# Kernel tuning notes

Hardware: AMD Instinct MI355X
Metric: run time of the kernel (lower is better)

The kernel has to match this reference:

```python
import jax, jax.numpy as jnp
import numpy as np

WS, WS2, UP = 8, 16, 2
DIM, HEADS = 192, 6
HD = DIM // HEADS
SCALE = HD ** -0.5
EPS = 1e-5

def _rel_index():
    r1, c1 = np.meshgrid(np.arange(WS), np.arange(WS), indexing='ij')
    r2, c2 = np.meshgrid(np.arange(WS2), np.arange(WS2), indexing='ij')
    r1, c1 = r1.ravel(), c1.ravel()          # 64 query positions
    r2, c2 = r2.ravel(), c2.ravel()          # 256 kv positions
    rel_row = r1[:, None] - r2[None, :]
    rel_col = c1[:, None] - c2[None, :]
    off = WS * UP - 1    # 15
    span = WS + WS * UP - 1  # 23
    return jnp.asarray((rel_row + off) * span + (rel_col + off))  # (64, 256)

REL_IDX = _rel_index()

def layer_norm(x, w, b):
    m = x.mean(-1, keepdims=True)
    v = ((x - m) ** 2).mean(-1, keepdims=True)
    return (x - m) * jax.lax.rsqrt(v + EPS) * w + b

def window_partition(x, ws):
    B, H, W, C = x.shape
    x = x.reshape(B, H // ws, ws, W // ws, ws, C).transpose(0, 1, 3, 2, 4, 5)
    return x.reshape(-1, ws * ws, C)

def window_reverse(w, ws, H, W, B):
    x = w.reshape(B, H // ws, W // ws, ws, ws, -1).transpose(0, 1, 3, 2, 4, 5)
    return x.reshape(B, H, W, -1)

def setup_inputs() -> dict:
    key = jax.random.key(0)
    ks = jax.random.split(key, 8)
    B, H, W, H2, W2 = 4, 128, 128, 256, 256
    s = 0.02
    return {
        'x': jax.random.normal(ks[0], (B, H * W, DIM), jnp.float32),
        'x2': jax.random.normal(ks[1], (B, H2 * W2, DIM), jnp.float32),
        'norm1_w': jnp.ones((DIM,), jnp.float32),
        'norm1_b': jnp.zeros((DIM,), jnp.float32),
        'qkv_w': jax.random.normal(ks[2], (DIM, DIM), jnp.float32) * s,
        'qkv_b': jnp.zeros((DIM,), jnp.float32),
        'qkv2_w': jax.random.normal(ks[3], (2 * DIM, DIM), jnp.float32) * s,
        'qkv2_b': jnp.zeros((2 * DIM,), jnp.float32),
        'rel_bias': jax.random.normal(ks[4], (23 * 23, HEADS), jnp.float32) * s,
        'proj_w': jax.random.normal(ks[5], (DIM, DIM), jnp.float32) * s,
        'proj_b': jnp.zeros((DIM,), jnp.float32),
        'norm2_w': jnp.ones((DIM,), jnp.float32),
        'norm2_b': jnp.zeros((DIM,), jnp.float32),
        'fc1_w': jax.random.normal(ks[6], (4 * DIM, DIM), jnp.float32) * s,
        'fc1_b': jnp.zeros((4 * DIM,), jnp.float32),
        'fc2_w': jax.random.normal(ks[7], (DIM, 4 * DIM), jnp.float32) * s,
        'fc2_b': jnp.zeros((DIM,), jnp.float32),
        'H': 128, 'W': 128, 'H2': 256, 'W2': 256,
    }

def reference(x, x2, norm1_w, norm1_b, qkv_w, qkv_b, qkv2_w, qkv2_b, rel_bias,
              proj_w, proj_b, norm2_w, norm2_b, fc1_w, fc1_b, fc2_w, fc2_b,
              H, W, H2, W2):
    B, L, C = x.shape
    shortcut = x
    xn = layer_norm(x, norm1_w, norm1_b).reshape(B, H, W, C)
    x2r = x2.reshape(B, H2, W2, C)

    xw = window_partition(xn, WS)      # (nW, 64, C)
    x2w = window_partition(x2r, WS2)   # (nW, 256, C)

    q = (xw @ qkv_w.T + qkv_b).reshape(-1, WS * WS, HEADS, HD).transpose(0, 2, 1, 3)
    kv = (x2w @ qkv2_w.T + qkv2_b).reshape(-1, WS2 * WS2, 2, HEADS, HD).transpose(2, 0, 3, 1, 4)
    k, v = kv[0], kv[1]                # (nW, h, 256, d)

    attn = jnp.einsum('whnd,whmd->whnm', q * SCALE, k)   # (nW, h, 64, 256)
    bias = rel_bias[REL_IDX]                             # (64, 256, h)
    attn = attn + bias.transpose(2, 0, 1)[None]
    attn = jax.nn.softmax(attn, axis=-1)
    out = jnp.einsum('whnm,whmd->wnhd', attn, v).reshape(-1, WS * WS, C)
    out = out @ proj_w.T + proj_b

    x = shortcut + window_reverse(out, WS, H, W, B).reshape(B, H * W, C)
    h = layer_norm(x, norm2_w, norm2_b)
    h = jax.nn.gelu(h @ fc1_w.T + fc1_b, approximate=False)
    x = x + (h @ fc2_w.T + fc2_b)
    return x
```

## Files before the change

kernel.cpp:

```cpp
#include <hip/hip_runtime.h>
#include <hip/hip_bf16.h>
#include <math.h>

typedef unsigned int u32;
typedef unsigned short u16;

typedef __attribute__((ext_vector_type(8))) short bf16x8;
typedef __attribute__((ext_vector_type(4))) float f32x4;

__device__ __forceinline__ float bflo(u32 u){ union{u32 i; float f;} c; c.i = u << 16; return c.f; }
__device__ __forceinline__ float bfhi(u32 u){ union{u32 i; float f;} c; c.i = u & 0xffff0000u; return c.f; }
__device__ __forceinline__ float bfs(u16 s){ union{u32 i; float f;} c; c.i = ((u32)s) << 16; return c.f; }
__device__ __forceinline__ u32 packbf(float a, float b){
  union{float f; u32 i;} ca, cb; ca.f = a; cb.f = b;
  u32 ua = (ca.i + 0x7fffu + ((ca.i >> 16) & 1u)) >> 16;
  u32 ub = (cb.i + 0x7fffu + ((cb.i >> 16) & 1u)) >> 16;
  return (ua & 0xffffu) | (ub << 16);
}
__device__ __forceinline__ u16 bf1(float a){
  union{float f; u32 i;} c; c.f = a;
  return (u16)((c.i + 0x7fffu + ((c.i >> 16) & 1u)) >> 16);
}
__device__ __forceinline__ bf16x8 pack8(float f0,float f1,float f2,float f3,
                                        float f4,float f5,float f6,float f7){
  union { u32 u[4]; bf16x8 v; } cv;
  cv.u[0]=packbf(f0,f1); cv.u[1]=packbf(f2,f3); cv.u[2]=packbf(f4,f5); cv.u[3]=packbf(f6,f7);
  return cv.v;
}
__device__ __forceinline__ float gelu_exact(float v){ return 0.5f*v*(1.0f + erff(v*0.70710678118654752f)); }
__device__ __forceinline__ bool detect_f32(const u32* rawn1){ return (rawn1[0] & 0xFFFFu) == 0u; }

#define SCALE_Q 0.17677669529663687f

#define P_N1W 0
#define P_N1B 192
#define P_N2W 384
#define P_N2B 576
#define P_QKVB 768
#define P_QKV2B 960
#define P_PROJB 1344
#define P_FC1B 1536
#define P_FC2B 2304
#define P_RELB 2496
#define P_TOTAL 5670
#define W_QKV 0
#define W_QKV2 18432
#define W_PROJ 55296
#define W_FC1 73728
#define W_FC2 147456
#define W_TOTAL 221184

__device__ __forceinline__ void stage_w64x192(const u32* __restrict__ src, u32* lds, int tid){
  #pragma unroll
  for (int t = 0; t < 6; ++t) {
    int idx = tid + t*256;
    int j = idx / 24, seg = idx % 24;
    uint4 v = *(const uint4*)(src + (size_t)j*96 + seg*4);
    int byt = (j*384 + seg*16) ^ ((j&7)<<4);
    *(uint4*)((char*)lds + byt) = v;
  }
}
__device__ __forceinline__ void stage_w64x192_t512(const u32* __restrict__ src, u32* lds, int tid){
  #pragma unroll
  for (int t = 0; t < 3; ++t) {
    int idx = tid + t*512;
    int j = idx / 24, seg = idx % 24;
    uint4 v = *(const uint4*)(src + (size_t)j*96 + seg*4);
    int byt = (j*384 + seg*16) ^ ((j&7)<<4);
    *(uint4*)((char*)lds + byt) = v;
  }
}
__device__ __forceinline__ void stage_w192x64_t512(const u32* __restrict__ src, int ch, u32* lds, int tid){
  #pragma unroll
  for (int t = 0; t < 3; ++t) {
    int idx = tid + t*512;
    int j = idx / 8, seg = idx % 8;
    uint4 v = *(const uint4*)(src + (size_t)j*384 + ch*32 + seg*4);
    int byt = (j*128 + seg*16) ^ ((j&7)<<4);
    *(uint4*)((char*)lds + byt) = v;
  }
}
__device__ __forceinline__ bf16x8 lds_w64(const u32* lds, int j, int kt, int g){
  int byt = (j*384 + kt*64 + g*16) ^ ((j&7)<<4);
  return *(const bf16x8*)((const char*)lds + byt);
}
__device__ __forceinline__ bf16x8 lds_w192(const u32* lds, int j, int kk, int g){
  int byt = (j*128 + kk*64 + g*16) ^ ((j&7)<<4);
  return *(const bf16x8*)((const char*)lds + byt);
}

__global__ __launch_bounds__(256) void k_canon_w(
    const void* qkvw, const void* qkv2w, const void* projw,
    const void* fc1w, const void* fc2w, const u32* rawn1, u32* cw)
{
  int idx = blockIdx.x*256 + threadIdx.x;
  bool isf32 = detect_f32(rawn1);
  const void* src; int off;
  if      (idx < W_QKV2){ src=qkvw;  off=idx; }
  else if (idx < W_PROJ){ src=qkv2w; off=idx-W_QKV2; }
  else if (idx < W_FC1) { src=projw; off=idx-W_PROJ; }
  else if (idx < W_FC2) { src=fc1w;  off=idx-W_FC1; }
  else                  { src=fc2w;  off=idx-W_FC2; }
  u32 o;
  if (isf32) { float2 v = ((const float2*)src)[off]; o = packbf(v.x, v.y); }
  else       { o = ((const u32*)src)[off]; }
  cw[idx] = o;
}

__global__ __launch_bounds__(256) void k_canon_v(
    const void* n1w, const void* n1b, const void* n2w, const void* n2b,
    const void* qkvb, const void* qkv2b, const void* projb,
    const void* fc1b, const void* fc2b, const void* relb,
    const u32* rawn1, float* par)
{
  int idx = blockIdx.x*256 + threadIdx.x;
  if (idx >= P_TOTAL) return;
  bool isf32 = detect_f32(rawn1);
  const void* src; int off;
  if      (idx < P_N1B)  { src=n1w;  off=idx; }
  else if (idx < P_N2W)  { src=n1b;  off=idx-P_N1B; }
  else if (idx < P_N2B)  { src=n2w;  off=idx-P_N2W; }
  else if (idx < P_QKVB) { src=n2b;  off=idx-P_N2B; }
  else if (idx < P_QKV2B){ src=qkvb; off=idx-P_QKVB; }
  else if (idx < P_PROJB){ src=qkv2b;off=idx-P_QKV2B; }
  else if (idx < P_FC1B) { src=projb;off=idx-P_PROJB; }
  else if (idx < P_FC2B) { src=fc1b; off=idx-P_FC1B; }
  else if (idx < P_RELB) { src=fc2b; off=idx-P_FC2B; }
  else                   { src=relb; off=idx-P_RELB; }
  par[idx] = isf32 ? ((const float*)src)[off] : bfs(((const u16*)src)[off]);
}

__global__ __launch_bounds__(256) void k_bias(
    const float* __restrict__ par, float* __restrict__ tbl)
{
  int idx = blockIdx.x*256 + threadIdx.x;
  int h  = idx >> 12;
  int remi = idx & 4095;
  int kt = remi >> 8;
  int qt = (remi >> 6) & 3;
  int ll = idx & 63;
  int lr = ll & 15, g = ll >> 4;
  int q = qt*16 + lr;
  int r1 = q >> 3, c1 = q & 7;
  float vv[4];
  #pragma unroll
  for (int i = 0; i < 4; ++i) {
    int kv = kt*16 + 4*g + i;
    int r2 = kv >> 4, c2 = kv & 15;
    vv[i] = par[P_RELB + ((r1-r2+15)*23 + (c1-c2+15))*6 + h];
  }
  ((float4*)tbl)[idx] = make_float4(vv[0], vv[1], vv[2], vv[3]);
}

__global__ __launch_bounds__(256) void k_qproj(
    const void* __restrict__ x, const u32* __restrict__ rawn1,
    const u32* __restrict__ cw, const float* __restrict__ par,
    u16* __restrict__ q_ws)
{
  __shared__ u32 wbuf[6144];
  int tid = threadIdx.x;
  int l = tid & 63, w = tid >> 6, lr = l & 15, g = l >> 4;
  int wi = blockIdx.x;
  int b = wi >> 8, rem = wi & 255, wh = rem >> 4, ww = rem & 15;
  bool isf32 = detect_f32(rawn1);

  bf16x8 a[6];
  {
    int t = w*16 + lr;
    int r = t >> 3, c = t & 7;
    size_t grow = (size_t)b*16384 + (size_t)(wh*8+r)*128 + (ww*8+c);
    float4 xf[12];
    if (isf32) {
      const float* xp = (const float*)x + grow*192;
      #pragma unroll
      for (int kt = 0; kt < 6; ++kt) {
        xf[kt*2]   = *(const float4*)(xp + kt*32 + 8*g);
        xf[kt*2+1] = *(const float4*)(xp + kt*32 + 8*g + 4);
      }
    } else {
      const u32* xp = (const u32*)x + grow*96;
      #pragma unroll
      for (int kt = 0; kt < 6; ++kt) {
        uint4 u = *(const uint4*)(xp + kt*16 + 4*g);
        xf[kt*2]   = make_float4(bflo(u.x), bfhi(u.x), bflo(u.y), bfhi(u.y));
        xf[kt*2+1] = make_float4(bflo(u.z), bfhi(u.z), bflo(u.w), bfhi(u.w));
      }
    }
    float s = 0.f, s2 = 0.f;
    #pragma unroll
    for (int q8 = 0; q8 < 12; ++q8) {
      s  += xf[q8].x + xf[q8].y + xf[q8].z + xf[q8].w;
      s2 += xf[q8].x*xf[q8].x + xf[q8].y*xf[q8].y + xf[q8].z*xf[q8].z + xf[q8].w*xf[q8].w;
    }
    s += __shfl_xor(s, 16); s2 += __shfl_xor(s2, 16);
    s += __shfl_xor(s, 32); s2 += __shfl_xor(s2, 32);
    float m = s * (1.f/192.f);
    float rstd = rsqrtf(s2*(1.f/192.f) - m*m + 1e-5f);
    #pragma unroll
    for (int kt = 0; kt < 6; ++kt) {
      int k0 = kt*32 + 8*g;
      float4 w0 = *(const float4*)(par + P_N1W + k0);
      float4 w1 = *(const float4*)(par + P_N1W + k0 + 4);
      float4 b0 = *(const float4*)(par + P_N1B + k0);
      float4 b1 = *(const float4*)(par + P_N1B + k0 + 4);
      float4 f0 = xf[kt*2], f1 = xf[kt*2+1];
      a[kt] = pack8((f0.x-m)*rstd*w0.x + b0.x, (f0.y-m)*rstd*w0.y + b0.y,
                    (f0.z-m)*rstd*w0.z + b0.z, (f0.w-m)*rstd*w0.w + b0.w,
                    (f1.x-m)*rstd*w1.x + b1.x, (f1.y-m)*rstd*w1.y + b1.y,
                    (f1.z-m)*rstd*w1.z + b1.z, (f1.w-m)*rstd*w1.w + b1.w);
    }
  }

  for (int ch = 0; ch < 3; ++ch) {
    __syncthreads();
    stage_w64x192(cw + W_QKV + (size_t)(ch*64)*96, wbuf, tid);
    __syncthreads();
    #pragma unroll
    for (int nt2 = 0; nt2 < 4; ++nt2) {
      int j = ch*64 + nt2*16 + lr;
      f32x4 acc = {0.f,0.f,0.f,0.f};
      #pragma unroll
      for (int kt = 0; kt < 6; ++kt) {
        bf16x8 bb = lds_w64(wbuf, nt2*16 + lr, kt, g);
        acc = __builtin_amdgcn_mfma_f32_16x16x32_bf16(a[kt], bb, acc, 0, 0, 0);
      }
      float bj = par[P_QKVB + j];
      int h = j >> 5, d = j & 31;
      #pragma unroll
      for (int i = 0; i < 4; ++i) {
        int n = w*16 + 4*g + i;
        q_ws[(size_t)(wi*6+h)*2048 + (size_t)n*32 + d] = bf1((acc[i] + bj) * SCALE_Q);
      }
    }
  }
}

__global__ __launch_bounds__(256) void k_kvproj(
    const void* __restrict__ x2, const u32* __restrict__ rawn1,
    const u32* __restrict__ cw, const float* __restrict__ par,
    u16* __restrict__ k_ws, u16* __restrict__ v_ws, int win0)
{
  __shared__ u32 wbuf[6144];
  int tid = threadIdx.x;
  int l = tid & 63, w = tid >> 6, lr = l & 15, g = l >> 4;
  int lwi = blockIdx.x >> 2, sub = blockIdx.x & 3;
  int wi = win0 + lwi;
  int b = wi >> 8, rem = wi & 255, wh = rem >> 4, ww = rem & 15;
  bool isf32 = detect_f32(rawn1);

  bf16x8 a[6];
  {
    int tt = sub*64 + w*16 + lr;
    int r = tt >> 4, c = tt & 15;
    size_t grow = (size_t)b*65536 + (size_t)(wh*16+r)*256 + (ww*16+c);
    if (isf32) {
      const float4* xp = (const float4*)x2 + grow*48;
      #pragma unroll
      for (int kt = 0; kt < 6; ++kt) {
        float4 f0 = xp[kt*8 + g*2];
        float4 f1 = xp[kt*8 + g*2 + 1];
        a[kt] = pack8(f0.x,f0.y,f0.z,f0.w, f1.x,f1.y,f1.z,f1.w);
      }
    } else {
      const u32* xp = (const u32*)x2 + grow*96;
      #pragma unroll
      for (int kt = 0; kt < 6; ++kt)
        a[kt] = *(const bf16x8*)(xp + kt*16 + g*4);
    }
  }

  for (int ch = 0; ch < 6; ++ch) {
    __syncthreads();
    stage_w64x192(cw + W_QKV2 + (size_t)(ch*64)*96, wbuf, tid);
    __syncthreads();
    if (ch < 3) {
      #pragma unroll
      for (int nt2 = 0; nt2 < 4; ++nt2) {
        int j = ch*64 + nt2*16 + lr;
        f32x4 acc = {0.f,0.f,0.f,0.f};
        #pragma unroll
        for (int kt = 0; kt < 6; ++kt) {
          bf16x8 bb = lds_w64(wbuf, nt2*16 + lr, kt, g);
          acc = __builtin_amdgcn_mfma_f32_16x16x32_bf16(a[kt], bb, acc, 0, 0, 0);
        }
        float bj = par[P_QKV2B + j];
        int h = j >> 5, d = j & 31;
        u16* dst = k_ws + (size_t)(lwi*6 + h)*8192 + d;
        #pragma unroll
        for (int i = 0; i < 4; ++i) {
          int tok = sub*64 + w*16 + 4*g + i;
          dst[(size_t)tok*32] = bf1(acc[i] + bj);
        }
      }
    } else {
      #pragma unroll
      for (int nt2 = 0; nt2 < 4; ++nt2) {
        f32x4 acc = {0.f,0.f,0.f,0.f};
        #pragma unroll
        for (int kt = 0; kt < 6; ++kt) {
          bf16x8 bb = lds_w64(wbuf, nt2*16 + lr, kt, g);
          acc = __builtin_amdgcn_mfma_f32_16x16x32_bf16(bb, a[kt], acc, 0, 0, 0);
        }
        int jr0 = (ch-3)*64 + nt2*16 + 4*g;
        int tok = sub*64 + w*16 + lr;
        #pragma unroll
        for (int i = 0; i < 4; ++i) {
          int jp = jr0 + i;
          int h = jp >> 5, dd = jp & 31;
          v_ws[(size_t)(lwi*6 + h)*8192 + (size_t)dd*256 + tok] = bf1(acc[i] + par[P_QKV2B + 192 + jp]);
        }
      }
    }
  }
}

__global__ __launch_bounds__(256) void k_attn(
    const u16* __restrict__ q_ws, const u16* __restrict__ k_ws,
    const u16* __restrict__ v_ws, const float* __restrict__ tbl,
    u16* __restrict__ O_ws, int win0)
{
  __shared__ u32 Psh[4*1024];
  __shared__ float msh[2][2][4];
  int tid = threadIdx.x;
  int w = tid >> 6, l = tid & 63;
  int lr = l & 15, g = l >> 4;
  int pairi = w >> 1, half = w & 1;
  int task = blockIdx.x*2 + pairi;
  int lwi = task / 6, h = task - lwi*6;
  int wi = win0 + lwi;

  bf16x8 qb[4];
  {
    const u16* qp = q_ws + (size_t)(wi*6+h)*2048;
    #pragma unroll
    for (int qt = 0; qt < 4; ++qt)
      qb[qt] = *(const bf16x8*)(qp + (qt*16 + lr)*32 + 8*g);
  }
  const u16* kp = k_ws + (size_t)(lwi*6+h)*8192;
  const u16* vp = v_ws + (size_t)(lwi*6+h)*8192;
  const float4* tb4 = (const float4*)tbl + (size_t)h*4096 + l;

  f32x4 ao[2][4];
  #pragma unroll
  for (int dt = 0; dt < 2; ++dt)
    #pragma unroll
    for (int qt = 0; qt < 4; ++qt) ao[dt][qt] = (f32x4){0.f,0.f,0.f,0.f};
  float mreg[4] = {-3.0e38f,-3.0e38f,-3.0e38f,-3.0e38f};
  float sreg[4] = {0.f,0.f,0.f,0.f};
  u32* pbu = Psh + w*1024;

  for (int ch = half*4; ch < half*4 + 4; ++ch) {
    bf16x8 ka0 = *(const bf16x8*)(kp + (2*ch)*512   + lr*32 + 8*g);
    bf16x8 ka1 = *(const bf16x8*)(kp + (2*ch+1)*512 + lr*32 + 8*g);
    f32x4 s0[4], s1[4];
    #pragma unroll
    for (int qt = 0; qt < 4; ++qt) {
      float4 b0 = tb4[(2*ch)*256   + qt*64];
      float4 b1 = tb4[(2*ch+1)*256 + qt*64];
      f32x4 c0; c0[0]=b0.x; c0[1]=b0.y; c0[2]=b0.z; c0[3]=b0.w;
      f32x4 c1; c1[0]=b1.x; c1[1]=b1.y; c1[2]=b1.z; c1[3]=b1.w;
      s0[qt] = __builtin_amdgcn_mfma_f32_16x16x32_bf16(ka0, qb[qt], c0, 0, 0, 0);
      s1[qt] = __builtin_amdgcn_mfma_f32_16x16x32_bf16(ka1, qb[qt], c1, 0, 0, 0);
    }
    #pragma unroll
    for (int qt = 0; qt < 4; ++qt) {
      float pm = fmaxf(fmaxf(fmaxf(s0[qt][0],s0[qt][1]), fmaxf(s0[qt][2],s0[qt][3])),
                       fmaxf(fmaxf(s1[qt][0],s1[qt][1]), fmaxf(s1[qt][2],s1[qt][3])));
      pm = fmaxf(pm, __shfl_xor(pm, 16));
      pm = fmaxf(pm, __shfl_xor(pm, 32));
      float nm = fmaxf(mreg[qt], pm);
      float resc = __expf(mreg[qt] - nm);
      mreg[qt] = nm;
      float p00 = __expf(s0[qt][0]-nm), p01 = __expf(s0[qt][1]-nm),
            p02 = __expf(s0[qt][2]-nm), p03 = __expf(s0[qt][3]-nm);
      float p10 = __expf(s1[qt][0]-nm), p11 = __expf(s1[qt][1]-nm),
            p12 = __expf(s1[qt][2]-nm), p13 = __expf(s1[qt][3]-nm);
      float ps = ((p00+p01)+(p02+p03)) + ((p10+p11)+(p12+p13));
      ps += __shfl_xor(ps, 16);
      ps += __shfl_xor(ps, 32);
      sreg[qt] = sreg[qt]*resc + ps;
      #pragma unroll
      for (int dt = 0; dt < 2; ++dt) {
        ao[dt][qt][0] *= resc; ao[dt][qt][1] *= resc;
        ao[dt][qt][2] *= resc; ao[dt][qt][3] *= resc;
      }
      int row = qt*16 + lr;
      int sw = (row & 3) << 2;
      *(uint2*)&pbu[row*16 + ((2*g) ^ sw)]     = make_uint2(packbf(p00,p01), packbf(p02,p03));
      *(uint2*)&pbu[row*16 + ((8 + 2*g) ^ sw)] = make_uint2(packbf(p10,p11), packbf(p12,p13));
    }
    asm volatile("" ::: "memory");
    bf16x8 va0 = *(const bf16x8*)(vp + lr*256        + ch*32 + 8*g);
    bf16x8 va1 = *(const bf16x8*)(vp + (16 + lr)*256 + ch*32 + 8*g);
    #pragma unroll
    for (int qt = 0; qt < 4; ++qt) {
      int row = qt*16 + lr;
      int sw = (row & 3) << 2;
      bf16x8 pa = *(const bf16x8*)&pbu[row*16 + ((4*g) ^ sw)];
      ao[0][qt] = __builtin_amdgcn_mfma_f32_16x16x32_bf16(va0, pa, ao[0][qt], 0, 0, 0);
      ao[1][qt] = __builtin_amdgcn_mfma_f32_16x16x32_bf16(va1, pa, ao[1][qt], 0, 0, 0);
    }
    asm volatile("" ::: "memory");
  }

  __syncthreads();
  if (half == 1) {
    float* dst = (float*)(Psh + pairi*2048);
    #pragma unroll
    for (int dt = 0; dt < 2; ++dt)
      #pragma unroll
      for (int qt = 0; qt < 4; ++qt)
        #pragma unroll
        for (int i = 0; i < 4; ++i)
          dst[(dt*16 + qt*4 + i)*64 + l] = ao[dt][qt][i];
    if (l == 0) {
      msh[pairi][0][0] = mreg[0]; msh[pairi][0][1] = mreg[1];
      msh[pairi][0][2] = mreg[2]; msh[pairi][0][3] = mreg[3];
      msh[pairi][1][0] = sreg[0]; msh[pairi][1][1] = sreg[1];
      msh[pairi][1][2] = sreg[2]; msh[pairi][1][3] = sreg[3];
    }
  }
  __syncthreads();
  if (half == 0) {
    const float* src = (const float*)(Psh + pairi*2048);
    #pragma unroll
    for (int qt = 0; qt < 4; ++qt) {
      float m1 = msh[pairi][0][qt], s1 = msh[pairi][1][qt];
      float M = fmaxf(mreg[qt], m1);
      float e0 = __expf(mreg[qt] - M), e1 = __expf(m1 - M);
      float rs = 1.0f / (sreg[qt]*e0 + s1*e1);
      u16* orow = O_ws + ((size_t)(wi*64) + qt*16 + lr)*192 + h*32;
      #pragma unroll
      for (int dt = 0; dt < 2; ++dt)
        #pragma unroll
        for (int i = 0; i < 4; ++i) {
          float o = ao[dt][qt][i]*e0 + src[(dt*16 + qt*4 + i)*64 + l]*e1;
          orow[dt*16 + 4*g + i] = bf1(o * rs);
        }
    }
  }
}

__global__ __launch_bounds__(256) void k_proj(
    const u16* __restrict__ O_ws, const u32* __restrict__ cw,
    const float* __restrict__ par, const void* __restrict__ x,
    const u32* __restrict__ rawn1, float* __restrict__ xres)
{
  __shared__ u32 wbuf[6144];
  int wi = blockIdx.x;
  int b = wi >> 8, rem = wi & 255, wh = rem >> 4, ww = rem & 15;
  int tid = threadIdx.x;
  int l = tid & 63, w = tid >> 6, lr = l & 15, g = l >> 4;
  bool isf32 = detect_f32(rawn1);
  int t = w*16 + lr;
  const u16* op = O_ws + (size_t)(wi*64 + t)*192;
  bf16x8 a[6];
  #pragma unroll
  for (int kt = 0; kt < 6; ++kt) a[kt] = *(const bf16x8*)(op + kt*32 + 8*g);

  for (int ch = 0; ch < 3; ++ch) {
    __syncthreads();
    stage_w64x192(cw + W_PROJ + (size_t)(ch*64)*96, wbuf, tid);
    __syncthreads();
    #pragma unroll
    for (int nt2 = 0; nt2 < 4; ++nt2) {
      int j = ch*64 + nt2*16 + lr;
      f32x4 acc = {0.f,0.f,0.f,0.f};
      #pragma unroll
      for (int kt = 0; kt < 6; ++kt) {
        bf16x8 bb = lds_w64(wbuf, nt2*16 + lr, kt, g);
        acc = __builtin_amdgcn_mfma_f32_16x16x32_bf16(a[kt], bb, acc, 0, 0, 0);
      }
      float bj = par[P_PROJB + j];
      #pragma unroll
      for (int i = 0; i < 4; ++i) {
        int tok = w*16 + 4*g + i;
        int rr = tok >> 3, cc = tok & 7;
        size_t grow = (size_t)b*16384 + (size_t)(wh*8+rr)*128 + (ww*8+cc);
        float sres = isf32 ? ((const float*)x)[grow*192 + j]
                           : bfs(((const u16*)x)[grow*192 + j]);
        xres[grow*192 + j] = sres + acc[i] + bj;
      }
    }
  }
}

__global__ __launch_bounds__(512) void k_mlp(
    const float* __restrict__ xres, const u32* __restrict__ cw,
    const float* __restrict__ par, float* __restrict__ out)
{
  __shared__ u32 wbuf[6144];
  __shared__ u16 Hc[8][32][64];
  int tid = threadIdx.x;
  int l = tid & 63, w = tid >> 6;
  int lr = l & 15, g = l >> 4;
  size_t row0 = (size_t)blockIdx.x * 256;

  bf16x8 a[2][6];
  #pragma unroll
  for (int mt = 0; mt < 2; ++mt) {
    size_t t = row0 + w*32 + mt*16 + lr;
    const float* xr = xres + t*192;
    float4 xf[12];
    #pragma unroll
    for (int kt = 0; kt < 6; ++kt) {
      xf[kt*2]   = *(const float4*)(xr + kt*32 + 8*g);
      xf[kt*2+1] = *(const float4*)(xr + kt*32 + 8*g + 4);
    }
    float s = 0.f, s2 = 0.f;
    #pragma unroll
    for (int q = 0; q < 12; ++q) {
      s  += xf[q].x + xf[q].y + xf[q].z + xf[q].w;
      s2 += xf[q].x*xf[q].x + xf[q].y*xf[q].y + xf[q].z*xf[q].z + xf[q].w*xf[q].w;
    }
    s += __shfl_xor(s, 16); s2 += __shfl_xor(s2, 16);
    s += __shfl_xor(s, 32); s2 += __shfl_xor(s2, 32);
    float m = s * (1.f/192.f);
    float rstd = rsqrtf(s2*(1.f/192.f) - m*m + 1e-5f);
    #pragma unroll
    for (int kt = 0; kt < 6; ++kt) {
      int k0 = kt*32 + 8*g;
      float4 w0 = *(const float4*)(par + P_N2W + k0);
      float4 w1 = *(const float4*)(par + P_N2W + k0 + 4);
      float4 b0 = *(const float4*)(par + P_N2B + k0);
      float4 b1 = *(const float4*)(par + P_N2B + k0 + 4);
      float4 f0 = xf[kt*2], f1 = xf[kt*2+1];
      a[mt][kt] = pack8((f0.x-m)*rstd*w0.x + b0.x, (f0.y-m)*rstd*w0.y + b0.y,
                        (f0.z-m)*rstd*w0.z + b0.z, (f0.w-m)*rstd*w0.w + b0.w,
                        (f1.x-m)*rstd*w1.x + b1.x, (f1.y-m)*rstd*w1.y + b1.y,
                        (f1.z-m)*rstd*w1.z + b1.z, (f1.w-m)*rstd*w1.w + b1.w);
    }
  }

  f32x4 acc2[2][12];
  #pragma unroll
  for (int mt = 0; mt < 2; ++mt)
    #pragma unroll
    for (int i = 0; i < 12; ++i) acc2[mt][i] = (f32x4){0.f,0.f,0.f,0.f};

  char* hbase = (char*)&Hc[w][0][0];
  for (int ch = 0; ch < 12; ++ch) {
    __syncthreads();
    stage_w64x192_t512(cw + W_FC1 + (size_t)(ch*64)*96, wbuf, tid);
    __syncthreads();
    #pragma unroll
    for (int nt2 = 0; nt2 < 4; ++nt2) {
      f32x4 acc0 = {0.f,0.f,0.f,0.f}, acc1 = {0.f,0.f,0.f,0.f};
      #pragma unroll
      for (int kt = 0; kt < 6; ++kt) {
        bf16x8 bb = lds_w64(wbuf, nt2*16 + lr, kt, g);
        acc0 = __builtin_amdgcn_mfma_f32_16x16x32_bf16(a[0][kt], bb, acc0, 0, 0, 0);
        acc1 = __builtin_amdgcn_mfma_f32_16x16x32_bf16(a[1][kt], bb, acc1, 0, 0, 0);
      }
      float bj = par[P_FC1B + ch*64 + nt2*16 + lr];
      #pragma unroll
      for (int mt = 0; mt < 2; ++mt) {
        f32x4 acc = mt ? acc1 : acc0;
        #pragma unroll
        for (int i = 0; i < 4; ++i) {
          int row = mt*16 + 4*g + i;
          int byt = (row*128 + (nt2*16+lr)*2) ^ ((row&7)<<4);
          *(u16*)(hbase + byt) = bf1(gelu_exact(acc[i] + bj));
        }
      }
    }
    __syncthreads();
    stage_w192x64_t512(cw + W_FC2, ch, wbuf, tid);
    __syncthreads();
    #pragma unroll
    for (int kk = 0; kk < 2; ++kk) {
      bf16x8 a20, a21;
      {
        int row0h = lr, row1h = 16 + lr;
        a20 = *(const bf16x8*)(hbase + ((row0h*128 + kk*64 + g*16) ^ ((row0h&7)<<4)));
        a21 = *(const bf16x8*)(hbase + ((row1h*128 + kk*64 + g*16) ^ ((row1h&7)<<4)));
      }
      #pragma unroll
      for (int nt = 0; nt < 12; ++nt) {
        bf16x8 bb = lds_w192(wbuf, nt*16 + lr, kk, g);
        acc2[0][nt] = __builtin_amdgcn_mfma_f32_16x16x32_bf16(a20, bb, acc2[0][nt], 0, 0, 0);
        acc2[1][nt] = __builtin_amdgcn_mfma_f32_16x16x32_bf16(a21, bb, acc2[1][nt], 0, 0, 0);
      }
    }
  }

  #pragma unroll
  for (int mt = 0; mt < 2; ++mt) {
    size_t trow = row0 + w*32 + mt*16 + 4*g;
    #pragma unroll
    for (int nt = 0; nt < 12; ++nt) {
      int j = nt*16 + lr;
      float bj = par[P_FC2B + j];
      #pragma unroll
      for (int i = 0; i < 4; ++i)
        out[(trow+i)*192 + j] = xres[(trow+i)*192 + j] + acc2[mt][nt][i] + bj;
    }
  }
}

extern "C" void kernel_launch(void* const* d_in, const int* in_sizes, int n_in,
                              void* d_out, int out_size, void* d_ws, size_t ws_size,
                              hipStream_t stream) {
  const void* x      = d_in[0];
  const void* x2     = d_in[1];
  const void* n1w    = d_in[2];
  const void* n1b    = d_in[3];
  const void* qkv_w  = d_in[4];
  const void* qkv_b  = d_in[5];
  const void* qkv2_w = d_in[6];
  const void* qkv2_b = d_in[7];
  const void* relb   = d_in[8];
  const void* proj_w = d_in[9];
  const void* proj_b = d_in[10];
  const void* n2w    = d_in[11];
  const void* n2b    = d_in[12];
  const void* fc1_w  = d_in[13];
  const void* fc1_b  = d_in[14];
  const void* fc2_w  = d_in[15];
  const void* fc2_b  = d_in[16];
  const u32* rawn1   = (const u32*)d_in[2];
  float* out = (float*)d_out;

  int nslice = (ws_size >= 202700000ull) ? 2 : 4;
  int nw = 1024 / nslice;
  size_t kvb = (size_t)nw * 98304;

  char* ws = (char*)d_ws;
  u16*   q_ws = (u16*)ws;
  u16*   k_ws = (u16*)(ws + 25165824);
  u16*   v_ws = (u16*)(ws + 25165824 + kvb);
  u16*   O_ws = (u16*)(ws + 25165824 + 2*kvb);
  float* xres = (float*)(ws + 50331648 + 2*kvb);
  u32*   cw   = (u32*)(ws + 100663296 + 2*kvb);
  float* tbl  = (float*)(ws + 100663296 + 2*kvb + 884736);
  float* par  = (float*)(ws + 100663296 + 2*kvb + 884736 + 393216);

  k_canon_w<<<W_TOTAL/256, 256, 0, stream>>>(qkv_w, qkv2_w, proj_w, fc1_w, fc2_w, rawn1, cw);
  k_canon_v<<<(P_TOTAL+255)/256, 256, 0, stream>>>(n1w, n1b, n2w, n2b, qkv_b, qkv2_b,
                                                   proj_b, fc1_b, fc2_b, relb, rawn1, par);
  k_bias  <<<96, 256, 0, stream>>>(par, tbl);
  k_qproj <<<1024, 256, 0, stream>>>(x, rawn1, cw, par, q_ws);
  for (int s = 0; s < nslice; ++s) {
    int win0 = s*nw;
    k_kvproj<<<nw*4, 256, 0, stream>>>(x2, rawn1, cw, par, k_ws, v_ws, win0);
    k_attn  <<<nw*3, 256, 0, stream>>>(q_ws, k_ws, v_ws, tbl, O_ws, win0);
  }
  k_proj  <<<1024, 256, 0, stream>>>(O_ws, cw, par, x, rawn1, xres);
  k_mlp   <<< 256, 512, 0, stream>>>(xres, cw, par, out);
}
```

Before: 648.7 us.

## Double-buffer MLP weight chunks with async global-to-LDS loads

The MLP kernel now uses two LDS weight buffers and issues direct global-to-LDS loads (global_load_lds) so the fc2 chunk loads while fc1 MFMAs run, and the next fc1 chunk loads while fc2 MFMAs run. The swizzle is folded into the global address so the LDS layout stays the same. This removes two barriers per chunk and the register round trip of staging. It raises LDS use by 24KB, which may lower occupancy, and it relies on the barrier placement being enough to wait for the async loads to finish.

```diff
diff --git a/kernel.cpp b/kernel.cpp
--- a/kernel.cpp
+++ b/kernel.cpp
@@ -60,26 +60,6 @@
     *(uint4*)((char*)lds + byt) = v;
   }
 }
-__device__ __forceinline__ void stage_w64x192_t512(const u32* __restrict__ src, u32* lds, int tid){
-  #pragma unroll
-  for (int t = 0; t < 3; ++t) {
-    int idx = tid + t*512;
-    int j = idx / 24, seg = idx % 24;
-    uint4 v = *(const uint4*)(src + (size_t)j*96 + seg*4);
-    int byt = (j*384 + seg*16) ^ ((j&7)<<4);
-    *(uint4*)((char*)lds + byt) = v;
-  }
-}
-__device__ __forceinline__ void stage_w192x64_t512(const u32* __restrict__ src, int ch, u32* lds, int tid){
-  #pragma unroll
-  for (int t = 0; t < 3; ++t) {
-    int idx = tid + t*512;
-    int j = idx / 8, seg = idx % 8;
-    uint4 v = *(const uint4*)(src + (size_t)j*384 + ch*32 + seg*4);
-    int byt = (j*128 + seg*16) ^ ((j&7)<<4);
-    *(uint4*)((char*)lds + byt) = v;
-  }
-}
 __device__ __forceinline__ bf16x8 lds_w64(const u32* lds, int j, int kt, int g){
   int byt = (j*384 + kt*64 + g*16) ^ ((j&7)<<4);
   return *(const bf16x8*)((const char*)lds + byt);
@@ -87,6 +67,36 @@
 __device__ __forceinline__ bf16x8 lds_w192(const u32* lds, int j, int kk, int g){
   int byt = (j*128 + kk*64 + g*16) ^ ((j&7)<<4);
   return *(const bf16x8*)((const char*)lds + byt);
+}
+
+typedef __attribute__((address_space(1))) const u32 gas_u32c;
+typedef __attribute__((address_space(3))) u32 las_u32;
+__device__ __forceinline__ void gld_lds16(const u32* g, u32* l){
+  gas_u32c* gp = (gas_u32c*)(unsigned long long)(size_t)g;
+  las_u32*  lp = (las_u32*)(unsigned int)(size_t)l;
+  __builtin_amdgcn_global_load_lds(gp, lp, 16, 0, 0);
+}
+__device__ __forceinline__ void issue_w64x192(const u32* src, u32* lds, int w, int l){
+  #pragma unroll
+  for (int t = 0; t < 3; ++t) {
+    int seg = w + t*8;
+    int a = seg*1024 + l*16;
+    int j = a / 384;
+    int off = a - j*384;
+    const u32* g = src + (size_t)j*96 + ((off ^ ((j&7)<<4)) >> 2);
+    gld_lds16(g, lds + seg*256);
+  }
+}
+__device__ __forceinline__ void issue_w192x64(const u32* src, int ch, u32* lds, int w, int l){
+  #pragma unroll
+  for (int t = 0; t < 3; ++t) {
+    int seg = w + t*8;
+    int a = seg*1024 + l*16;
+    int j = a >> 7;
+    int off = a & 127;
+    const u32* g = src + (size_t)j*384 + ch*32 + ((off ^ ((j&7)<<4)) >> 2);
+    gld_lds16(g, lds + seg*256);
+  }
 }
 
 __global__ __launch_bounds__(256) void k_canon_w(
@@ -489,7 +499,8 @@
     const float* __restrict__ xres, const u32* __restrict__ cw,
     const float* __restrict__ par, float* __restrict__ out)
 {
-  __shared__ u32 wbuf[6144];
+  __shared__ u32 wbufA[6144];
+  __shared__ u32 wbufB[6144];
   __shared__ u16 Hc[8][32][64];
   int tid = threadIdx.x;
   int l = tid & 63, w = tid >> 6;
@@ -539,16 +550,20 @@
     for (int i = 0; i < 12; ++i) acc2[mt][i] = (f32x4){0.f,0.f,0.f,0.f};
 
   char* hbase = (char*)&Hc[w][0][0];
+  const u32* w1p = cw + W_FC1;
+  const u32* w2p = cw + W_FC2;
+
+  issue_w64x192(w1p, wbufA, w, l);
+  __syncthreads();
+
   for (int ch = 0; ch < 12; ++ch) {
-    __syncthreads();
-    stage_w64x192_t512(cw + W_FC1 + (size_t)(ch*64)*96, wbuf, tid);
-    __syncthreads();
+    issue_w192x64(w2p, ch, wbufB, w, l);
     #pragma unroll
     for (int nt2 = 0; nt2 < 4; ++nt2) {
       f32x4 acc0 = {0.f,0.f,0.f,0.f}, acc1 = {0.f,0.f,0.f,0.f};
       #pragma unroll
       for (int kt = 0; kt < 6; ++kt) {
-        bf16x8 bb = lds_w64(wbuf, nt2*16 + lr, kt, g);
+        bf16x8 bb = lds_w64(wbufA, nt2*16 + lr, kt, g);
         acc0 = __builtin_amdgcn_mfma_f32_16x16x32_bf16(a[0][kt], bb, acc0, 0, 0, 0);
         acc1 = __builtin_amdgcn_mfma_f32_16x16x32_bf16(a[1][kt], bb, acc1, 0, 0, 0);
       }
@@ -565,8 +580,7 @@
       }
     }
     __syncthreads();
-    stage_w192x64_t512(cw + W_FC2, ch, wbuf, tid);
-    __syncthreads();
+    if (ch < 11) issue_w64x192(w1p + (size_t)((ch+1)*64)*96, wbufA, w, l);
     #pragma unroll
     for (int kk = 0; kk < 2; ++kk) {
       bf16x8 a20, a21;
@@ -577,11 +591,12 @@
       }
       #pragma unroll
       for (int nt = 0; nt < 12; ++nt) {
-        bf16x8 bb = lds_w192(wbuf, nt*16 + lr, kk, g);
+        bf16x8 bb = lds_w192(wbufB, nt*16 + lr, kk, g);
         acc2[0][nt] = __builtin_amdgcn_mfma_f32_16x16x32_bf16(a20, bb, acc2[0][nt], 0, 0, 0);
         acc2[1][nt] = __builtin_amdgcn_mfma_f32_16x16x32_bf16(a21, bb, acc2[1][nt], 0, 0, 0);
       }
     }
+    __syncthreads();
   }
 
   #pragma unroll
```

After: 630.8 us. 1.03x faster.
